# Performance work log

Hardware: AMD Instinct MI355X
Metric: run time of the kernel (lower is better)

Reference implementation:

```python
import jax, jax.numpy as jnp
import numpy as np

P = 16         # patch size
D = 192        # embed dim (vit_tiny)
NH = 3         # heads
DEPTH = 12
HID = 768      # mlp hidden = 4*D
NCLS = 1000
PCT = 0.25
EPS = 1e-6


def _ln(x, s, b):
    m = x.mean(-1, keepdims=True)
    v = ((x - m) ** 2).mean(-1, keepdims=True)
    return (x - m) * jax.lax.rsqrt(v + EPS) * s + b


def setup_inputs() -> dict:
    key = jax.random.key(0)
    ks = jax.random.split(key, 24)
    B, IMG = 64, 384
    std = 0.02
    d = {
        "magno_image": jax.random.normal(ks[0], (B, 3, IMG, IMG), jnp.float32),
        "line_drawing": jax.random.uniform(ks[1], (B, 1, IMG, IMG), jnp.float32),
        "conv_w": jax.random.normal(ks[2], (D, 3, P, P), jnp.float32) * std,
        "conv_b": jnp.zeros((D,), jnp.float32),
        "pos_embed": jax.random.normal(ks[3], (1, (IMG // P) ** 2 + 1, D), jnp.float32) * std,
        "cls_token": jax.random.normal(ks[4], (1, 1, D), jnp.float32) * std,
        "ln1_s": jnp.ones((DEPTH, D), jnp.float32),
        "ln1_b": jnp.zeros((DEPTH, D), jnp.float32),
        "qkv_w": jax.random.normal(ks[5], (DEPTH, D, 3 * D), jnp.float32) * std,
        "qkv_b": jnp.zeros((DEPTH, 3 * D), jnp.float32),
        "proj_w": jax.random.normal(ks[6], (DEPTH, D, D), jnp.float32) * std,
        "proj_b": jnp.zeros((DEPTH, D), jnp.float32),
        "ln2_s": jnp.ones((DEPTH, D), jnp.float32),
        "ln2_b": jnp.zeros((DEPTH, D), jnp.float32),
        "fc1_w": jax.random.normal(ks[7], (DEPTH, D, HID), jnp.float32) * std,
        "fc1_b": jnp.zeros((DEPTH, HID), jnp.float32),
        "fc2_w": jax.random.normal(ks[8], (DEPTH, HID, D), jnp.float32) * std,
        "fc2_b": jnp.zeros((DEPTH, D), jnp.float32),
        "normf_s": jnp.ones((D,), jnp.float32),
        "normf_b": jnp.zeros((D,), jnp.float32),
        "head_w": jax.random.normal(ks[9], (D, NCLS), jnp.float32) * std,
        "head_b": jnp.zeros((NCLS,), jnp.float32),
    }
    return d


def _forward(magno_image, line_drawing, conv_w, conv_b, pos_embed, cls_token,
             ln1_s, ln1_b, qkv_w, qkv_b, proj_w, proj_b, ln2_s, ln2_b,
             fc1_w, fc1_b, fc2_w, fc2_b, normf_s, normf_b, head_w, head_b):
    B, _, IMG, _ = magno_image.shape
    g = IMG // P
    N = g * g
    k = int(N * PCT)
    hd = D // NH

    # --- PatchImportanceScorer: avg-pool(patch_size) then flatten ---
    scores = line_drawing.reshape(B, g, P, g, P).mean(axis=(2, 4)).reshape(B, N)

    # --- patch embed (conv stride == kernel == reshaped matmul) ---
    x = magno_image.reshape(B, 3, g, P, g, P).transpose(0, 2, 4, 1, 3, 5)
    patches = x.reshape(B, N, 3 * P * P) @ conv_w.reshape(D, 3 * P * P).T + conv_b

    # --- top_k selection + gather of patches and pos-embed ---
    _, idx = jax.lax.top_k(scores, k)                      # (B, k)
    sel = jnp.take_along_axis(patches, idx[:, :, None], axis=1)
    pos = jnp.take_along_axis(
        jnp.broadcast_to(pos_embed[:, 1:, :], (B, N, D)), idx[:, :, None], axis=1)
    sel = sel + pos

    cls = jnp.broadcast_to(cls_token + pos_embed[:, :1, :], (B, 1, D))
    seq = jnp.concatenate([cls, sel], axis=1)              # (B, 1+k, D)
    S = 1 + k

    def block(h, p):
        l1s, l1b, qw, qb, pw, pb, l2s, l2b, f1w, f1b, f2w, f2b = p
        y = _ln(h, l1s, l1b)
        qkv = (y @ qw + qb).reshape(B, S, 3, NH, hd)
        q, kk, v = qkv[:, :, 0], qkv[:, :, 1], qkv[:, :, 2]  # (B,S,NH,hd)
        att = jnp.einsum('bqhd,bkhd->bhqk', q, kk) / np.sqrt(hd).astype(np.float32)
        att = jax.nn.softmax(att, axis=-1)
        o = jnp.einsum('bhqk,bkhd->bqhd', att, v).reshape(B, S, D)
        h = h + o @ pw + pb
        y = _ln(h, l2s, l2b)
        h = h + jax.nn.gelu(y @ f1w + f1b, approximate=False) @ f2w + f2b
        return h, None

    seq, _ = jax.lax.scan(block, seq, (ln1_s, ln1_b, qkv_w, qkv_b, proj_w, proj_b,
                                       ln2_s, ln2_b, fc1_w, fc1_b, fc2_w, fc2_b))
    seq = _ln(seq, normf_s, normf_b)
    return seq[:, 0] @ head_w + head_b


def reference(magno_image, line_drawing, conv_w, conv_b, pos_embed, cls_token,
              ln1_s, ln1_b, qkv_w, qkv_b, proj_w, proj_b, ln2_s, ln2_b,
              fc1_w, fc1_b, fc2_w, fc2_b, normf_s, normf_b, head_w, head_b):
    return _forward(magno_image, line_drawing, conv_w, conv_b, pos_embed, cls_token,
                    ln1_s, ln1_b, qkv_w, qkv_b, proj_w, proj_b, ln2_s, ln2_b,
                    fc1_w, fc1_b, fc2_w, fc2_b, normf_s, normf_b, head_w, head_b)
```

## Files before the change

kernel.cpp:

```cpp
#include <hip/hip_runtime.h>
#include <hip/hip_bf16.h>
#include <cmath>


#define Bsz   64
#define NPATCH 576
#define KSEL  144
#define SEQ   145
#define DIM   192
#define HIDN  768

typedef __bf16 bf16x8 __attribute__((ext_vector_type(8)));
typedef float  f32x4  __attribute__((ext_vector_type(4)));

__global__ __launch_bounds__(256) void scores_kernel(const float* __restrict__ line,
                                                     float* __restrict__ scores)
{
    int gp = blockIdx.x;
    int b = gp / NPATCH, p = gp % NPATCH;
    int gy = p / 24, gx = p % 24;
    int t = threadIdx.x, py = t >> 4, px = t & 15;
    float v = line[((size_t)b * 384 + gy * 16 + py) * 384 + gx * 16 + px];
    for (int off = 32; off; off >>= 1) v += __shfl_xor(v, off);
    __shared__ float red[4];
    if ((t & 63) == 0) red[t >> 6] = v;
    __syncthreads();
    if (t == 0) scores[gp] = (red[0] + red[1] + red[2] + red[3]) * (1.f / 256.f);
}

__global__ __launch_bounds__(256) void topk_kernel(const float* __restrict__ scores,
                                                   int* __restrict__ idx)
{
    int b = blockIdx.x;
    __shared__ float s[NPATCH];
    for (int i = threadIdx.x; i < NPATCH; i += 256) s[i] = scores[b * NPATCH + i];
    __syncthreads();
    for (int i = threadIdx.x; i < NPATCH; i += 256) {
        float si = s[i];
        int cnt = 0;
        for (int j = 0; j < NPATCH; ++j) {
            float sj = s[j];
            cnt += (sj > si) || (sj == si && j < i);
        }
        if (cnt < KSEL) idx[b * KSEL + cnt] = i;
    }
}

__global__ __launch_bounds__(256) void gather_kernel(const float* __restrict__ magno,
                                                     const int* __restrict__ idx,
                                                     __hip_bfloat16* __restrict__ selp)
{
    int bs = blockIdx.x;
    int b = bs / KSEL;
    int pi = idx[bs];
    int gy = pi / 24, gx = pi % 24;
    int t = threadIdx.x, py = t >> 4, px = t & 15;
    size_t src = ((size_t)b * 3 * 384 + gy * 16 + py) * 384 + gx * 16 + px;
    __hip_bfloat16* dst = &selp[(size_t)bs * 768];
#pragma unroll
    for (int c = 0; c < 3; ++c)
        dst[c * 256 + t] = __float2bfloat16(magno[src + (size_t)c * 384 * 384]);
}

__global__ __launch_bounds__(256) void convert_bf16_kernel(const float* __restrict__ src,
                                                           __hip_bfloat16* __restrict__ dst,
                                                           int n)
{
    int i = blockIdx.x * 256 + threadIdx.x;
    if (i < n) dst[i] = __float2bfloat16(src[i]);
}

__global__ __launch_bounds__(256) void transpose_w_kernel(const float* __restrict__ src,
                                                          __hip_bfloat16* __restrict__ dst,
                                                          int R, int C)
{
    __shared__ float t[32][33];
    size_t lo = (size_t)blockIdx.z * R * C;
    int r0 = blockIdx.y * 32, c0 = blockIdx.x * 32;
    int tx = threadIdx.x & 31, ty = threadIdx.x >> 5;
#pragma unroll
    for (int i = 0; i < 32; i += 8)
        t[ty + i][tx] = src[lo + (size_t)(r0 + ty + i) * C + c0 + tx];
    __syncthreads();
#pragma unroll
    for (int i = 0; i < 32; i += 8)
        dst[lo + (size_t)(c0 + ty + i) * R + r0 + tx] = __float2bfloat16(t[tx][ty + i]);
}

__global__ void cls_kernel(const float* __restrict__ cls, const float* __restrict__ pos,
                           float* __restrict__ h)
{
    int b = blockIdx.x, t = threadIdx.x;
    h[(size_t)b * SEQ * DIM + t] = cls[t] + pos[t];
}

__global__ __launch_bounds__(256) void ln_kernel(const float* __restrict__ x,
                                                 const float* __restrict__ s,
                                                 const float* __restrict__ bia,
                                                 __hip_bfloat16* __restrict__ y, int ntok)
{
    int w = threadIdx.x >> 6, lane = threadIdx.x & 63;
    int tok = blockIdx.x * 4 + w;
    if (tok >= ntok) return;
    const float* xp = &x[(size_t)tok * DIM];
    float x0 = xp[lane], x1 = xp[lane + 64], x2 = xp[lane + 128];
    float sum = x0 + x1 + x2;
    for (int off = 32; off; off >>= 1) sum += __shfl_xor(sum, off);
    float mean = sum * (1.f / 192.f);
    float d0 = x0 - mean, d1 = x1 - mean, d2 = x2 - mean;
    float vs = d0 * d0 + d1 * d1 + d2 * d2;
    for (int off = 32; off; off >>= 1) vs += __shfl_xor(vs, off);
    float rs = rsqrtf(vs * (1.f / 192.f) + 1e-6f);
    __hip_bfloat16* yp = &y[(size_t)tok * DIM];
    yp[lane]       = __float2bfloat16(d0 * rs * s[lane]       + bia[lane]);
    yp[lane + 64]  = __float2bfloat16(d1 * rs * s[lane + 64]  + bia[lane + 64]);
    yp[lane + 128] = __float2bfloat16(d2 * rs * s[lane + 128] + bia[lane + 128]);
}

template <int MODE>
__global__ __launch_bounds__(256) void gemm_bf16(const __hip_bfloat16* __restrict__ A,
                                                 const __hip_bfloat16* __restrict__ Wt,
                                                 const float* __restrict__ bias,
                                                 void* __restrict__ Cout,
                                                 int M, int N, int K,
                                                 const int* __restrict__ selidx,
                                                 const float* __restrict__ pos)
{
    __shared__ __align__(16) char As[8192];
    __shared__ __align__(16) char Bs[8192];
    const int tid = threadIdx.x;
    const int lane = tid & 63, wid = tid >> 6;
    const int wr = wid >> 1, wc = wid & 1;
    const int lr = lane & 15, lk = lane >> 4;
    const int m0 = blockIdx.y * 64, n0 = blockIdx.x * 64;
    f32x4 acc[2][2] = {};

    for (int k0 = 0; k0 < K; k0 += 64) {
#pragma unroll
        for (int it = 0; it < 2; ++it) {
            int chunk = it * 256 + tid;
            int r = chunk >> 3, g = chunk & 7;
            int loff = r * 128 + ((g ^ (r & 7)) * 16);
            *reinterpret_cast<uint4*>(As + loff) =
                *reinterpret_cast<const uint4*>(&A[(size_t)(m0 + r) * K + k0 + g * 8]);
            *reinterpret_cast<uint4*>(Bs + loff) =
                *reinterpret_cast<const uint4*>(&Wt[(size_t)(n0 + r) * K + k0 + g * 8]);
        }
        __syncthreads();
#pragma unroll
        for (int kc = 0; kc < 2; ++kc) {
            int g = kc * 4 + lk;
            bf16x8 af[2], bfr[2];
#pragma unroll
            for (int mi = 0; mi < 2; ++mi) {
                int r = wr * 32 + mi * 16 + lr;
                af[mi] = *reinterpret_cast<const bf16x8*>(As + r * 128 + ((g ^ (r & 7)) * 16));
            }
#pragma unroll
            for (int ni = 0; ni < 2; ++ni) {
                int r = wc * 32 + ni * 16 + lr;
                bfr[ni] = *reinterpret_cast<const bf16x8*>(Bs + r * 128 + ((g ^ (r & 7)) * 16));
            }
#pragma unroll
            for (int mi = 0; mi < 2; ++mi)
#pragma unroll
                for (int ni = 0; ni < 2; ++ni)
                    acc[mi][ni] = __builtin_amdgcn_mfma_f32_16x16x32_bf16(
                        af[mi], bfr[ni], acc[mi][ni], 0, 0, 0);
        }
        __syncthreads();
    }

#pragma unroll
    for (int mi = 0; mi < 2; ++mi)
#pragma unroll
    for (int ni = 0; ni < 2; ++ni)
#pragma unroll
    for (int j = 0; j < 4; ++j) {
        int row = m0 + wr * 32 + mi * 16 + (lane >> 4) * 4 + j;
        int col = n0 + wc * 32 + ni * 16 + (lane & 15);
        float v = acc[mi][ni][j] + bias[col];
        if (MODE == 2) {
            ((__hip_bfloat16*)Cout)[(size_t)row * N + col] =
                __float2bfloat16(0.5f * v * (1.f + erff(v * 0.70710678118654752f)));
        } else {
            int bb2 = row / KSEL, ss = row % KSEL;
            int pi = selidx[row];
            v += pos[(size_t)(1 + pi) * DIM + col];
            ((float*)Cout)[((size_t)bb2 * SEQ + 1 + ss) * DIM + col] = v;
        }
    }
}

__global__ __launch_bounds__(256) void gemm_qkv(const __hip_bfloat16* __restrict__ A,
                                                const __hip_bfloat16* __restrict__ Wt,
                                                const float* __restrict__ bias,
                                                __hip_bfloat16* __restrict__ qk,
                                                __hip_bfloat16* __restrict__ Vt)
{
    __shared__ __align__(16) char As[8192];
    __shared__ __align__(16) char Bs[8192];
    const int tid = threadIdx.x;
    const int lane = tid & 63, wid = tid >> 6;
    const int wr = wid >> 1, wc = wid & 1;
    const int lr = lane & 15, lk = lane >> 4;
    const int m0 = blockIdx.y * 64, n0 = blockIdx.x * 64;
    const int K = DIM;
    f32x4 acc[2][2] = {};

    for (int k0 = 0; k0 < K; k0 += 64) {
#pragma unroll
        for (int it = 0; it < 2; ++it) {
            int chunk = it * 256 + tid;
            int r = chunk >> 3, g = chunk & 7;
            int loff = r * 128 + ((g ^ (r & 7)) * 16);
            *reinterpret_cast<uint4*>(As + loff) =
                *reinterpret_cast<const uint4*>(&A[(size_t)(m0 + r) * K + k0 + g * 8]);
            *reinterpret_cast<uint4*>(Bs + loff) =
                *reinterpret_cast<const uint4*>(&Wt[(size_t)(n0 + r) * K + k0 + g * 8]);
        }
        __syncthreads();
#pragma unroll
        for (int kc = 0; kc < 2; ++kc) {
            int g = kc * 4 + lk;
            bf16x8 af[2], bfr[2];
#pragma unroll
            for (int mi = 0; mi < 2; ++mi) {
                int r = wr * 32 + mi * 16 + lr;
                af[mi] = *reinterpret_cast<const bf16x8*>(As + r * 128 + ((g ^ (r & 7)) * 16));
            }
#pragma unroll
            for (int ni = 0; ni < 2; ++ni) {
                int r = wc * 32 + ni * 16 + lr;
                bfr[ni] = *reinterpret_cast<const bf16x8*>(Bs + r * 128 + ((g ^ (r & 7)) * 16));
            }
#pragma unroll
            for (int mi = 0; mi < 2; ++mi)
#pragma unroll
                for (int ni = 0; ni < 2; ++ni)
                    acc[mi][ni] = __builtin_amdgcn_mfma_f32_16x16x32_bf16(
                        af[mi], bfr[ni], acc[mi][ni], 0, 0, 0);
        }
        __syncthreads();
    }

#pragma unroll
    for (int mi = 0; mi < 2; ++mi)
#pragma unroll
    for (int ni = 0; ni < 2; ++ni)
#pragma unroll
    for (int j = 0; j < 4; ++j) {
        int row = m0 + wr * 32 + mi * 16 + (lane >> 4) * 4 + j;
        int col = n0 + wc * 32 + ni * 16 + (lane & 15);
        float v = acc[mi][ni][j] + bias[col];
        if (col < 384) {
            qk[(size_t)row * 384 + col] = __float2bfloat16(v);
        } else {
            int c = col - 384;
            int b = row / SEQ, s = row - b * SEQ;
            Vt[((size_t)(b * 3 + (c >> 6)) * 64 + (c & 63)) * 160 + s] = __float2bfloat16(v);
        }
    }
}

__global__ __launch_bounds__(256) void attnproj_kernel(const __hip_bfloat16* __restrict__ qk,
                                                       const __hip_bfloat16* __restrict__ Vt,
                                                       const __hip_bfloat16* __restrict__ Wp,
                                                       const float* __restrict__ pbias,
                                                       float* __restrict__ h,
                                                       const float* __restrict__ ls,
                                                       const float* __restrict__ lb,
                                                       __hip_bfloat16* __restrict__ y)
{
    const int b = blockIdx.y, qt = blockIdx.x;
    const int tid = threadIdx.x;
    const int w = tid >> 6, lane = tid & 63;
    const int lr = lane & 15, lg = lane >> 4;
    __shared__ __hip_bfloat16 Ps[3][32][168];
    __shared__ __hip_bfloat16 Ot[32][200];
    __shared__ float redsum[4][32];
    __shared__ float redsq[4][32];

    const size_t qbase = (size_t)b * SEQ * 384;
    const int q0 = qt * 32;

    if (w < 3) {
        const int hh = w;
        bf16x8 aq[2][2];
#pragma unroll
        for (int mi = 0; mi < 2; ++mi)
#pragma unroll
            for (int ks = 0; ks < 2; ++ks)
                aq[mi][ks] = *reinterpret_cast<const bf16x8*>(
                    &qk[qbase + (size_t)(q0 + mi * 16 + lr) * 384 + hh * 64 + ks * 32 + lg * 8]);
        f32x4 sc[2][10];
#pragma unroll
        for (int mi = 0; mi < 2; ++mi)
#pragma unroll
            for (int nf = 0; nf < 10; ++nf) sc[mi][nf] = (f32x4){0.f, 0.f, 0.f, 0.f};
#pragma unroll
        for (int nf = 0; nf < 10; ++nf) {
            int key = nf * 16 + lr;
#pragma unroll
            for (int ks = 0; ks < 2; ++ks) {
                bf16x8 bk = *reinterpret_cast<const bf16x8*>(
                    &qk[qbase + (size_t)key * 384 + 192 + hh * 64 + ks * 32 + lg * 8]);
#pragma unroll
                for (int mi = 0; mi < 2; ++mi)
                    sc[mi][nf] = __builtin_amdgcn_mfma_f32_16x16x32_bf16(
                        aq[mi][ks], bk, sc[mi][nf], 0, 0, 0);
            }
        }
#pragma unroll
        for (int mi = 0; mi < 2; ++mi) {
            float mx[4] = {-1e30f, -1e30f, -1e30f, -1e30f};
#pragma unroll
            for (int nf = 0; nf < 10; ++nf) {
                bool valid = nf * 16 + lr < SEQ;
#pragma unroll
                for (int j = 0; j < 4; ++j) {
                    float v = valid ? sc[mi][nf][j] * 0.125f : -1e30f;
                    sc[mi][nf][j] = v;
                    mx[j] = fmaxf(mx[j], v);
                }
            }
#pragma unroll
            for (int j = 0; j < 4; ++j)
                for (int off = 1; off < 16; off <<= 1)
                    mx[j] = fmaxf(mx[j], __shfl_xor(mx[j], off));
            float sm[4] = {0.f, 0.f, 0.f, 0.f};
#pragma unroll
            for (int nf = 0; nf < 10; ++nf)
#pragma unroll
                for (int j = 0; j < 4; ++j) {
                    float p = __expf(sc[mi][nf][j] - mx[j]);
                    sc[mi][nf][j] = p;
                    sm[j] += p;
                }
#pragma unroll
            for (int j = 0; j < 4; ++j) {
                for (int off = 1; off < 16; off <<= 1) sm[j] += __shfl_xor(sm[j], off);
                sm[j] = 1.f / sm[j];
            }
#pragma unroll
            for (int nf = 0; nf < 10; ++nf) {
                int key = nf * 16 + lr;
#pragma unroll
                for (int j = 0; j < 4; ++j)
                    Ps[hh][mi * 16 + lg * 4 + j][key] = __float2bfloat16(sc[mi][nf][j] * sm[j]);
            }
        }
        const __hip_bfloat16* vtb = &Vt[(size_t)(b * 3 + hh) * 64 * 160];
        f32x4 oacc[2][4];
#pragma unroll
        for (int mi = 0; mi < 2; ++mi)
#pragma unroll
            for (int nf = 0; nf < 4; ++nf) oacc[mi][nf] = (f32x4){0.f, 0.f, 0.f, 0.f};
#pragma unroll
        for (int ks = 0; ks < 5; ++ks) {
            bf16x8 ap[2];
            ap[0] = *reinterpret_cast<const bf16x8*>(&Ps[hh][lr][ks * 32 + lg * 8]);
            ap[1] = *reinterpret_cast<const bf16x8*>(&Ps[hh][16 + lr][ks * 32 + lg * 8]);
#pragma unroll
            for (int nf = 0; nf < 4; ++nf) {
                bf16x8 bv = *reinterpret_cast<const bf16x8*>(
                    &vtb[(size_t)(nf * 16 + lr) * 160 + ks * 32 + lg * 8]);
#pragma unroll
                for (int mi = 0; mi < 2; ++mi)
                    oacc[mi][nf] = __builtin_amdgcn_mfma_f32_16x16x32_bf16(
                        ap[mi], bv, oacc[mi][nf], 0, 0, 0);
            }
        }
#pragma unroll
        for (int mi = 0; mi < 2; ++mi)
#pragma unroll
            for (int nf = 0; nf < 4; ++nf)
#pragma unroll
                for (int j = 0; j < 4; ++j)
                    Ot[mi * 16 + lg * 4 + j][hh * 64 + nf * 16 + lr] =
                        __float2bfloat16(oacc[mi][nf][j]);
    }
    __syncthreads();

    f32x4 pacc[2][3];
#pragma unroll
    for (int mi = 0; mi < 2; ++mi)
#pragma unroll
        for (int nf = 0; nf < 3; ++nf) pacc[mi][nf] = (f32x4){0.f, 0.f, 0.f, 0.f};
#pragma unroll
    for (int kk = 0; kk < 6; ++kk) {
        bf16x8 af[2];
        af[0] = *reinterpret_cast<const bf16x8*>(&Ot[lr][kk * 32 + lg * 8]);
        af[1] = *reinterpret_cast<const bf16x8*>(&Ot[16 + lr][kk * 32 + lg * 8]);
#pragma unroll
        for (int nf = 0; nf < 3; ++nf) {
            int ncol = w * 48 + nf * 16 + lr;
            bf16x8 bw = *reinterpret_cast<const bf16x8*>(&Wp[(size_t)ncol * 192 + kk * 32 + lg * 8]);
#pragma unroll
            for (int mi = 0; mi < 2; ++mi)
                pacc[mi][nf] = __builtin_amdgcn_mfma_f32_16x16x32_bf16(
                    af[mi], bw, pacc[mi][nf], 0, 0, 0);
        }
    }
    float v[2][3][4];
    float psum[2][4] = {}, psq[2][4] = {};
#pragma unroll
    for (int mi = 0; mi < 2; ++mi)
#pragma unroll
    for (int nf = 0; nf < 3; ++nf) {
        int col = w * 48 + nf * 16 + lr;
        float bcol = pbias[col];
#pragma unroll
        for (int j = 0; j < 4; ++j) {
            int q = q0 + mi * 16 + lg * 4 + j;
            float res = (q < SEQ) ? h[((size_t)b * SEQ + q) * DIM + col] : 0.f;
            float t = pacc[mi][nf][j] + bcol + res;
            v[mi][nf][j] = t;
            psum[mi][j] += t;
            psq[mi][j] += t * t;
        }
    }
#pragma unroll
    for (int mi = 0; mi < 2; ++mi)
#pragma unroll
        for (int j = 0; j < 4; ++j) {
            for (int off = 1; off < 16; off <<= 1) {
                psum[mi][j] += __shfl_xor(psum[mi][j], off);
                psq[mi][j]  += __shfl_xor(psq[mi][j], off);
            }
            redsum[w][mi * 16 + lg * 4 + j] = psum[mi][j];
            redsq[w][mi * 16 + lg * 4 + j]  = psq[mi][j];
        }
    __syncthreads();
#pragma unroll
    for (int mi = 0; mi < 2; ++mi) {
#pragma unroll
        for (int j = 0; j < 4; ++j) {
            int r = mi * 16 + lg * 4 + j;
            int q = q0 + r;
            if (q >= SEQ) continue;
            float tsum = redsum[0][r] + redsum[1][r] + redsum[2][r] + redsum[3][r];
            float tsq  = redsq[0][r]  + redsq[1][r]  + redsq[2][r]  + redsq[3][r];
            float mean = tsum * (1.f / 192.f);
            float var  = tsq * (1.f / 192.f) - mean * mean;
            float rs = rsqrtf(var + 1e-6f);
#pragma unroll
            for (int nf = 0; nf < 3; ++nf) {
                int col = w * 48 + nf * 16 + lr;
                float t = v[mi][nf][j];
                h[((size_t)b * SEQ + q) * DIM + col] = t;
                y[((size_t)b * SEQ + q) * DIM + col] =
                    __float2bfloat16((t - mean) * rs * ls[col] + lb[col]);
            }
        }
    }
}

template <bool DO_LN>
__global__ __launch_bounds__(256) void gemm_res_ln32(const __hip_bfloat16* __restrict__ A,
                                                     const __hip_bfloat16* __restrict__ Wt,
                                                     const float* __restrict__ bias,
                                                     float* __restrict__ h,
                                                     const float* __restrict__ ls,
                                                     const float* __restrict__ lb,
                                                     __hip_bfloat16* __restrict__ y)
{
    __shared__ __align__(16) char As[4096];
    __shared__ __align__(16) char Bs[24576];
    __shared__ float redsum[2][32];
    __shared__ float redsq[2][32];
    const int tid = threadIdx.x;
    const int lane = tid & 63, w = tid >> 6;
    const int wm = w & 1, wn = w >> 1;
    const int lr = lane & 15, lg = lane >> 4;
    const int m0 = blockIdx.x * 32;
    const int K = HIDN;
    f32x4 acc[6] = {};

    for (int k0 = 0; k0 < K; k0 += 64) {
        {
            int r = tid >> 3, g = tid & 7;
            *reinterpret_cast<uint4*>(As + r * 128 + ((g ^ (r & 7)) * 16)) =
                *reinterpret_cast<const uint4*>(&A[(size_t)(m0 + r) * K + k0 + g * 8]);
        }
        {
            int chunk = tid;
#pragma unroll
            for (int it = 0; it < 6; ++it, chunk += 256) {
                int r = chunk >> 3, g = chunk & 7;
                *reinterpret_cast<uint4*>(Bs + r * 128 + ((g ^ (r & 7)) * 16)) =
                    *reinterpret_cast<const uint4*>(&Wt[(size_t)r * K + k0 + g * 8]);
            }
        }
        __syncthreads();
#pragma unroll
        for (int kc = 0; kc < 2; ++kc) {
            int g = kc * 4 + lg;
            int ar = wm * 16 + lr;
            bf16x8 af = *reinterpret_cast<const bf16x8*>(As + ar * 128 + ((g ^ (ar & 7)) * 16));
#pragma unroll
            for (int nf = 0; nf < 6; ++nf) {
                int br = wn * 96 + nf * 16 + lr;
                bf16x8 bfv = *reinterpret_cast<const bf16x8*>(Bs + br * 128 + ((g ^ (br & 7)) * 16));
                acc[nf] = __builtin_amdgcn_mfma_f32_16x16x32_bf16(af, bfv, acc[nf], 0, 0, 0);
            }
        }
        __syncthreads();
    }

    float v[6][4];
    float sum[4] = {0.f, 0.f, 0.f, 0.f}, sq[4] = {0.f, 0.f, 0.f, 0.f};
#pragma unroll
    for (int nf = 0; nf < 6; ++nf) {
        int col = wn * 96 + nf * 16 + lr;
        float bcol = bias[col];
#pragma unroll
        for (int j = 0; j < 4; ++j) {
            int row = m0 + wm * 16 + lg * 4 + j;
            float t = acc[nf][j] + bcol + h[(size_t)row * DIM + col];
            v[nf][j] = t;
            sum[j] += t;
            sq[j] += t * t;
        }
    }
    if (DO_LN) {
#pragma unroll
        for (int j = 0; j < 4; ++j) {
            for (int off = 1; off < 16; off <<= 1) {
                sum[j] += __shfl_xor(sum[j], off);
                sq[j]  += __shfl_xor(sq[j], off);
            }
            if (lr == 0) {
                redsum[wn][wm * 16 + lg * 4 + j] = sum[j];
                redsq[wn][wm * 16 + lg * 4 + j]  = sq[j];
            }
        }
        __syncthreads();
#pragma unroll
        for (int j = 0; j < 4; ++j) {
            int r = wm * 16 + lg * 4 + j;
            int row = m0 + r;
            float tsum = redsum[0][r] + redsum[1][r];
            float tsq  = redsq[0][r]  + redsq[1][r];
            float mean = tsum * (1.f / 192.f);
            float var  = tsq * (1.f / 192.f) - mean * mean;
            float rs = rsqrtf(var + 1e-6f);
#pragma unroll
            for (int nf = 0; nf < 6; ++nf) {
                int col = wn * 96 + nf * 16 + lr;
                float t = v[nf][j];
                h[(size_t)row * DIM + col] = t;
                y[(size_t)row * DIM + col] =
                    __float2bfloat16((t - mean) * rs * ls[col] + lb[col]);
            }
        }
    } else {
#pragma unroll
        for (int nf = 0; nf < 6; ++nf) {
            int col = wn * 96 + nf * 16 + lr;
#pragma unroll
            for (int j = 0; j < 4; ++j) {
                int row = m0 + wm * 16 + lg * 4 + j;
                h[(size_t)row * DIM + col] = v[nf][j];
            }
        }
    }
}

__global__ __launch_bounds__(256) void head_kernel(const float* __restrict__ h,
                                                   const float* __restrict__ nfs,
                                                   const float* __restrict__ nfb,
                                                   const float* __restrict__ hw,
                                                   const float* __restrict__ hb,
                                                   float* __restrict__ out)
{
    int b = blockIdx.x, t = threadIdx.x;
    __shared__ float y[DIM];
    __shared__ float red[4];
    float x = (t < DIM) ? h[(size_t)b * SEQ * DIM + t] : 0.f;
    float sum = x;
    for (int off = 32; off; off >>= 1) sum += __shfl_xor(sum, off);
    if ((t & 63) == 0) red[t >> 6] = sum;
    __syncthreads();
    float mean = (red[0] + red[1] + red[2] + red[3]) * (1.f / 192.f);
    __syncthreads();
    float d = (t < DIM) ? (x - mean) : 0.f;
    float v = d * d;
    for (int off = 32; off; off >>= 1) v += __shfl_xor(v, off);
    if ((t & 63) == 0) red[t >> 6] = v;
    __syncthreads();
    float var = (red[0] + red[1] + red[2] + red[3]) * (1.f / 192.f);
    float rs = rsqrtf(var + 1e-6f);
    if (t < DIM) y[t] = d * rs * nfs[t] + nfb[t];
    __syncthreads();
    for (int n = t; n < 1000; n += 256) {
        float acc = hb[n];
#pragma unroll 8
        for (int k = 0; k < DIM; ++k)
            acc = fmaf(y[k], hw[(size_t)k * 1000 + n], acc);
        out[(size_t)b * 1000 + n] = acc;
    }
}

extern "C" void kernel_launch(void* const* d_in, const int* in_sizes, int n_in,
                              void* d_out, int out_size, void* d_ws, size_t ws_size,
                              hipStream_t stream)
{
    const float* magno  = (const float*)d_in[0];
    const float* line   = (const float*)d_in[1];
    const float* conv_w = (const float*)d_in[2];
    const float* conv_b = (const float*)d_in[3];
    const float* pos    = (const float*)d_in[4];
    const float* cls    = (const float*)d_in[5];
    const float* ln1_s  = (const float*)d_in[6];
    const float* ln1_b  = (const float*)d_in[7];
    const float* qkv_w  = (const float*)d_in[8];
    const float* qkv_b  = (const float*)d_in[9];
    const float* proj_w = (const float*)d_in[10];
    const float* proj_b = (const float*)d_in[11];
    const float* ln2_s  = (const float*)d_in[12];
    const float* ln2_b  = (const float*)d_in[13];
    const float* fc1_w  = (const float*)d_in[14];
    const float* fc1_b  = (const float*)d_in[15];
    const float* fc2_w  = (const float*)d_in[16];
    const float* fc2_b  = (const float*)d_in[17];
    const float* normf_s = (const float*)d_in[18];
    const float* normf_b = (const float*)d_in[19];
    const float* head_w = (const float*)d_in[20];
    const float* head_b = (const float*)d_in[21];
    float* out = (float*)d_out;
    (void)in_sizes; (void)n_in; (void)out_size; (void)ws_size;

    char* ws = (char*)d_ws;
    int*            idx     = (int*)            (ws + 0);
    float*          h       = (float*)          (ws + 147456);
    __hip_bfloat16* y       = (__hip_bfloat16*) (ws + 7274496);
    __hip_bfloat16* qk      = (__hip_bfloat16*) (ws + 10838016);
    __hip_bfloat16* Vt      = (__hip_bfloat16*) (ws + 17965056);
    __hip_bfloat16* tbuf    = (__hip_bfloat16*) (ws + 21897216);
    __hip_bfloat16* wt_qkv  = (__hip_bfloat16*) (ws + 36151296);
    __hip_bfloat16* wt_proj = (__hip_bfloat16*) (ws + 38805504);
    __hip_bfloat16* wt_fc1  = (__hip_bfloat16*) (ws + 39690240);
    __hip_bfloat16* wt_fc2  = (__hip_bfloat16*) (ws + 43229184);
    float*          scoresbuf = (float*)qk;
    __hip_bfloat16* convT     = y;
    __hip_bfloat16* selp      = tbuf;

    hipMemsetAsync(Vt, 0, 3932160, stream);
    transpose_w_kernel<<<dim3(18, 6, 12), 256, 0, stream>>>(qkv_w, wt_qkv, DIM, 576);
    transpose_w_kernel<<<dim3(6, 6, 12),  256, 0, stream>>>(proj_w, wt_proj, DIM, DIM);
    transpose_w_kernel<<<dim3(24, 6, 12), 256, 0, stream>>>(fc1_w, wt_fc1, DIM, HIDN);
    transpose_w_kernel<<<dim3(6, 24, 12), 256, 0, stream>>>(fc2_w, wt_fc2, HIDN, DIM);
    convert_bf16_kernel<<<576, 256, 0, stream>>>(conv_w, convT, DIM * 768);

    scores_kernel<<<Bsz * NPATCH, 256, 0, stream>>>(line, scoresbuf);
    topk_kernel<<<Bsz, 256, 0, stream>>>(scoresbuf, idx);
    gather_kernel<<<Bsz * KSEL, 256, 0, stream>>>(magno, idx, selp);
    cls_kernel<<<Bsz, DIM, 0, stream>>>(cls, pos, h);
    gemm_bf16<3><<<dim3(3, 144), 256, 0, stream>>>(selp, convT, conv_b, h,
                                                   9216, DIM, 768, idx, pos);

    const int ntok = Bsz * SEQ;
    ln_kernel<<<ntok / 4, 256, 0, stream>>>(h, ln1_s, ln1_b, y, ntok);
    for (int l = 0; l < 12; ++l) {
        gemm_qkv<<<dim3(9, 145), 256, 0, stream>>>(y, wt_qkv + (size_t)l * 576 * DIM,
                                                   qkv_b + l * 576, qk, Vt);
        attnproj_kernel<<<dim3(5, Bsz), 256, 0, stream>>>(qk, Vt,
                                                          wt_proj + (size_t)l * DIM * DIM,
                                                          proj_b + l * DIM, h,
                                                          ln2_s + l * DIM, ln2_b + l * DIM, y);
        gemm_bf16<2><<<dim3(12, 145), 256, 0, stream>>>(y, wt_fc1 + (size_t)l * HIDN * DIM,
                                                        fc1_b + l * HIDN, tbuf,
                                                        ntok, HIDN, DIM, nullptr, nullptr);
        if (l < 11)
            gemm_res_ln32<true><<<ntok / 32, 256, 0, stream>>>(
                tbuf, wt_fc2 + (size_t)l * DIM * HIDN, fc2_b + l * DIM, h,
                ln1_s + (l + 1) * DIM, ln1_b + (l + 1) * DIM, y);
        else
            gemm_res_ln32<false><<<ntok / 32, 256, 0, stream>>>(
                tbuf, wt_fc2 + (size_t)l * DIM * HIDN, fc2_b + l * DIM, h,
                nullptr, nullptr, y);
    }
    head_kernel<<<Bsz, 256, 0, stream>>>(h, normf_s, normf_b, head_w, head_b, out);
}
```

Measured before the change: 1.136 ms.

## Widen attention and fc2 residual-LN kernels to 512 threads with retiled work

The attention+projection kernel now runs 8 waves instead of 4. Each of the 6 attention waves handles one head and one 16-query half, and the projection is split 2x4 across all 8 waves. The fc2 GEMM with residual and LayerNorm now uses 64-row tiles, 512 threads and a 128-wide K step, which cuts the grid from 290 to 145 blocks. The goal is more parallel waves per block and fewer redundant weight loads per row. The cost is larger shared-memory use (about 64KB) and lower block count, which may limit occupancy on the CUs.

```diff
diff --git a/kernel.cpp b/kernel.cpp
--- a/kernel.cpp
+++ b/kernel.cpp
@@ -263,7 +263,7 @@
     }
 }
 
-__global__ __launch_bounds__(256) void attnproj_kernel(const __hip_bfloat16* __restrict__ qk,
+__global__ __launch_bounds__(512) void attnproj_kernel(const __hip_bfloat16* __restrict__ qk,
                                                        const __hip_bfloat16* __restrict__ Vt,
                                                        const __hip_bfloat16* __restrict__ Wp,
                                                        const float* __restrict__ pbias,
@@ -284,20 +284,15 @@
     const size_t qbase = (size_t)b * SEQ * 384;
     const int q0 = qt * 32;
 
-    if (w < 3) {
-        const int hh = w;
-        bf16x8 aq[2][2];
-#pragma unroll
-        for (int mi = 0; mi < 2; ++mi)
-#pragma unroll
-            for (int ks = 0; ks < 2; ++ks)
-                aq[mi][ks] = *reinterpret_cast<const bf16x8*>(
-                    &qk[qbase + (size_t)(q0 + mi * 16 + lr) * 384 + hh * 64 + ks * 32 + lg * 8]);
-        f32x4 sc[2][10];
-#pragma unroll
-        for (int mi = 0; mi < 2; ++mi)
-#pragma unroll
-            for (int nf = 0; nf < 10; ++nf) sc[mi][nf] = (f32x4){0.f, 0.f, 0.f, 0.f};
+    if (w < 6) {
+        const int hh = w >> 1, half = w & 1;
+        const int qrow = q0 + half * 16;
+        bf16x8 aq[2];
+#pragma unroll
+        for (int ks = 0; ks < 2; ++ks)
+            aq[ks] = *reinterpret_cast<const bf16x8*>(
+                &qk[qbase + (size_t)(qrow + lr) * 384 + hh * 64 + ks * 32 + lg * 8]);
+        f32x4 sc[10] = {};
 #pragma unroll
         for (int nf = 0; nf < 10; ++nf) {
             int key = nf * 16 + lr;
@@ -305,263 +300,248 @@
             for (int ks = 0; ks < 2; ++ks) {
                 bf16x8 bk = *reinterpret_cast<const bf16x8*>(
                     &qk[qbase + (size_t)key * 384 + 192 + hh * 64 + ks * 32 + lg * 8]);
-#pragma unroll
-                for (int mi = 0; mi < 2; ++mi)
-                    sc[mi][nf] = __builtin_amdgcn_mfma_f32_16x16x32_bf16(
-                        aq[mi][ks], bk, sc[mi][nf], 0, 0, 0);
-            }
-        }
-#pragma unroll
-        for (int mi = 0; mi < 2; ++mi) {
-            float mx[4] = {-1e30f, -1e30f, -1e30f, -1e30f};
-#pragma unroll
-            for (int nf = 0; nf < 10; ++nf) {
-                bool valid = nf * 16 + lr < SEQ;
-#pragma unroll
-                for (int j = 0; j < 4; ++j) {
-                    float v = valid ? sc[mi][nf][j] * 0.125f : -1e30f;
-                    sc[mi][nf][j] = v;
-                    mx[j] = fmaxf(mx[j], v);
-                }
-            }
+                sc[nf] = __builtin_amdgcn_mfma_f32_16x16x32_bf16(aq[ks], bk, sc[nf], 0, 0, 0);
+            }
+        }
+        float mx[4] = {-1e30f, -1e30f, -1e30f, -1e30f};
+#pragma unroll
+        for (int nf = 0; nf < 10; ++nf) {
+            bool valid = nf * 16 + lr < SEQ;
+#pragma unroll
+            for (int j = 0; j < 4; ++j) {
+                float v = valid ? sc[nf][j] * 0.125f : -1e30f;
+                sc[nf][j] = v;
+                mx[j] = fmaxf(mx[j], v);
+            }
+        }
+#pragma unroll
+        for (int j = 0; j < 4; ++j)
+            for (int off = 1; off < 16; off <<= 1)
+                mx[j] = fmaxf(mx[j], __shfl_xor(mx[j], off));
+        float sm[4] = {0.f, 0.f, 0.f, 0.f};
+#pragma unroll
+        for (int nf = 0; nf < 10; ++nf)
+#pragma unroll
+            for (int j = 0; j < 4; ++j) {
+                float p = __expf(sc[nf][j] - mx[j]);
+                sc[nf][j] = p;
+                sm[j] += p;
+            }
+#pragma unroll
+        for (int j = 0; j < 4; ++j) {
+            for (int off = 1; off < 16; off <<= 1) sm[j] += __shfl_xor(sm[j], off);
+            sm[j] = 1.f / sm[j];
+        }
+#pragma unroll
+        for (int nf = 0; nf < 10; ++nf) {
+            int key = nf * 16 + lr;
 #pragma unroll
             for (int j = 0; j < 4; ++j)
-                for (int off = 1; off < 16; off <<= 1)
-                    mx[j] = fmaxf(mx[j], __shfl_xor(mx[j], off));
-            float sm[4] = {0.f, 0.f, 0.f, 0.f};
-#pragma unroll
-            for (int nf = 0; nf < 10; ++nf)
-#pragma unroll
-                for (int j = 0; j < 4; ++j) {
-                    float p = __expf(sc[mi][nf][j] - mx[j]);
-                    sc[mi][nf][j] = p;
-                    sm[j] += p;
-                }
-#pragma unroll
-            for (int j = 0; j < 4; ++j) {
-                for (int off = 1; off < 16; off <<= 1) sm[j] += __shfl_xor(sm[j], off);
-                sm[j] = 1.f / sm[j];
-            }
-#pragma unroll
-            for (int nf = 0; nf < 10; ++nf) {
-                int key = nf * 16 + lr;
-#pragma unroll
-                for (int j = 0; j < 4; ++j)
-                    Ps[hh][mi * 16 + lg * 4 + j][key] = __float2bfloat16(sc[mi][nf][j] * sm[j]);
-            }
+                Ps[hh][half * 16 + lg * 4 + j][key] = __float2bfloat16(sc[nf][j] * sm[j]);
         }
         const __hip_bfloat16* vtb = &Vt[(size_t)(b * 3 + hh) * 64 * 160];
-        f32x4 oacc[2][4];
-#pragma unroll
-        for (int mi = 0; mi < 2; ++mi)
-#pragma unroll
-            for (int nf = 0; nf < 4; ++nf) oacc[mi][nf] = (f32x4){0.f, 0.f, 0.f, 0.f};
+        f32x4 oacc[4] = {};
 #pragma unroll
         for (int ks = 0; ks < 5; ++ks) {
-            bf16x8 ap[2];
-            ap[0] = *reinterpret_cast<const bf16x8*>(&Ps[hh][lr][ks * 32 + lg * 8]);
-            ap[1] = *reinterpret_cast<const bf16x8*>(&Ps[hh][16 + lr][ks * 32 + lg * 8]);
+            bf16x8 ap = *reinterpret_cast<const bf16x8*>(&Ps[hh][half * 16 + lr][ks * 32 + lg * 8]);
 #pragma unroll
             for (int nf = 0; nf < 4; ++nf) {
                 bf16x8 bv = *reinterpret_cast<const bf16x8*>(
                     &vtb[(size_t)(nf * 16 + lr) * 160 + ks * 32 + lg * 8]);
-#pragma unroll
-                for (int mi = 0; mi < 2; ++mi)
-                    oacc[mi][nf] = __builtin_amdgcn_mfma_f32_16x16x32_bf16(
-                        ap[mi], bv, oacc[mi][nf], 0, 0, 0);
-            }
-        }
-#pragma unroll
-        for (int mi = 0; mi < 2; ++mi)
-#pragma unroll
-            for (int nf = 0; nf < 4; ++nf)
-#pragma unroll
-                for (int j = 0; j < 4; ++j)
-                    Ot[mi * 16 + lg * 4 + j][hh * 64 + nf * 16 + lr] =
-                        __float2bfloat16(oacc[mi][nf][j]);
-    }
-    __syncthreads();
-
-    f32x4 pacc[2][3];
-#pragma unroll
-    for (int mi = 0; mi < 2; ++mi)
-#pragma unroll
-        for (int nf = 0; nf < 3; ++nf) pacc[mi][nf] = (f32x4){0.f, 0.f, 0.f, 0.f};
+                oacc[nf] = __builtin_amdgcn_mfma_f32_16x16x32_bf16(ap, bv, oacc[nf], 0, 0, 0);
+            }
+        }
+#pragma unroll
+        for (int nf = 0; nf < 4; ++nf)
+#pragma unroll
+            for (int j = 0; j < 4; ++j)
+                Ot[half * 16 + lg * 4 + j][hh * 64 + nf * 16 + lr] =
+                    __float2bfloat16(oacc[nf][j]);
+    }
+    __syncthreads();
+
+    const int wm = w & 1, wn = w >> 1;
+    f32x4 pacc[3] = {};
 #pragma unroll
     for (int kk = 0; kk < 6; ++kk) {
-        bf16x8 af[2];
-        af[0] = *reinterpret_cast<const bf16x8*>(&Ot[lr][kk * 32 + lg * 8]);
-        af[1] = *reinterpret_cast<const bf16x8*>(&Ot[16 + lr][kk * 32 + lg * 8]);
+        bf16x8 af = *reinterpret_cast<const bf16x8*>(&Ot[wm * 16 + lr][kk * 32 + lg * 8]);
 #pragma unroll
         for (int nf = 0; nf < 3; ++nf) {
-            int ncol = w * 48 + nf * 16 + lr;
+            int ncol = wn * 48 + nf * 16 + lr;
             bf16x8 bw = *reinterpret_cast<const bf16x8*>(&Wp[(size_t)ncol * 192 + kk * 32 + lg * 8]);
-#pragma unroll
-            for (int mi = 0; mi < 2; ++mi)
-                pacc[mi][nf] = __builtin_amdgcn_mfma_f32_16x16x32_bf16(
-                    af[mi], bw, pacc[mi][nf], 0, 0, 0);
-        }
-    }
-    float v[2][3][4];
-    float psum[2][4] = {}, psq[2][4] = {};
-#pragma unroll
-    for (int mi = 0; mi < 2; ++mi)
+            pacc[nf] = __builtin_amdgcn_mfma_f32_16x16x32_bf16(af, bw, pacc[nf], 0, 0, 0);
+        }
+    }
+    float v[3][4];
+    float psum[4] = {}, psq[4] = {};
 #pragma unroll
     for (int nf = 0; nf < 3; ++nf) {
-        int col = w * 48 + nf * 16 + lr;
+        int col = wn * 48 + nf * 16 + lr;
         float bcol = pbias[col];
 #pragma unroll
         for (int j = 0; j < 4; ++j) {
-            int q = q0 + mi * 16 + lg * 4 + j;
+            int q = q0 + wm * 16 + lg * 4 + j;
             float res = (q < SEQ) ? h[((size_t)b * SEQ + q) * DIM + col] : 0.f;
-            float t = pacc[mi][nf][j] + bcol + res;
-            v[mi][nf][j] = t;
-            psum[mi][j] += t;
-            psq[mi][j] += t * t;
-        }
-    }
-#pragma unroll
-    for (int mi = 0; mi < 2; ++mi)
-#pragma unroll
-        for (int j = 0; j < 4; ++j) {
-            for (int off = 1; off < 16; off <<= 1) {
-                psum[mi][j] += __shfl_xor(psum[mi][j], off);
-                psq[mi][j]  += __shfl_xor(psq[mi][j], off);
-            }
-            redsum[w][mi * 16 + lg * 4 + j] = psum[mi][j];
-            redsq[w][mi * 16 + lg * 4 + j]  = psq[mi][j];
-        }
-    __syncthreads();
-#pragma unroll
-    for (int mi = 0; mi < 2; ++mi) {
-#pragma unroll
-        for (int j = 0; j < 4; ++j) {
-            int r = mi * 16 + lg * 4 + j;
-            int q = q0 + r;
-            if (q >= SEQ) continue;
-            float tsum = redsum[0][r] + redsum[1][r] + redsum[2][r] + redsum[3][r];
-            float tsq  = redsq[0][r]  + redsq[1][r]  + redsq[2][r]  + redsq[3][r];
-            float mean = tsum * (1.f / 192.f);
-            float var  = tsq * (1.f / 192.f) - mean * mean;
-            float rs = rsqrtf(var + 1e-6f);
-#pragma unroll
-            for (int nf = 0; nf < 3; ++nf) {
-                int col = w * 48 + nf * 16 + lr;
-                float t = v[mi][nf][j];
-                h[((size_t)b * SEQ + q) * DIM + col] = t;
-                y[((size_t)b * SEQ + q) * DIM + col] =
-                    __float2bfloat16((t - mean) * rs * ls[col] + lb[col]);
-            }
+            float t = pacc[nf][j] + bcol + res;
+            v[nf][j] = t;
+            psum[j] += t;
+            psq[j] += t * t;
+        }
+    }
+#pragma unroll
+    for (int j = 0; j < 4; ++j) {
+        for (int off = 1; off < 16; off <<= 1) {
+            psum[j] += __shfl_xor(psum[j], off);
+            psq[j]  += __shfl_xor(psq[j], off);
+        }
+        if (lr == 0) {
+            redsum[wn][wm * 16 + lg * 4 + j] = psum[j];
+            redsq[wn][wm * 16 + lg * 4 + j]  = psq[j];
+        }
+    }
+    __syncthreads();
+#pragma unroll
+    for (int j = 0; j < 4; ++j) {
+        int r = wm * 16 + lg * 4 + j;
+        int q = q0 + r;
+        if (q >= SEQ) continue;
+        float tsum = redsum[0][r] + redsum[1][r] + redsum[2][r] + redsum[3][r];
+        float tsq  = redsq[0][r]  + redsq[1][r]  + redsq[2][r]  + redsq[3][r];
+        float mean = tsum * (1.f / 192.f);
+        float var  = tsq * (1.f / 192.f) - mean * mean;
+        float rs = rsqrtf(var + 1e-6f);
+#pragma unroll
+        for (int nf = 0; nf < 3; ++nf) {
+            int col = wn * 48 + nf * 16 + lr;
+            float t = v[nf][j];
+            h[((size_t)b * SEQ + q) * DIM + col] = t;
+            y[((size_t)b * SEQ + q) * DIM + col] =
+                __float2bfloat16((t - mean) * rs * ls[col] + lb[col]);
         }
     }
 }
 
 template <bool DO_LN>
-__global__ __launch_bounds__(256) void gemm_res_ln32(const __hip_bfloat16* __restrict__ A,
-                                                     const __hip_bfloat16* __restrict__ Wt,
-                                                     const float* __restrict__ bias,
-                                                     float* __restrict__ h,
-                                                     const float* __restrict__ ls,
-                                                     const float* __restrict__ lb,
-                                                     __hip_bfloat16* __restrict__ y)
-{
-    __shared__ __align__(16) char As[4096];
-    __shared__ __align__(16) char Bs[24576];
-    __shared__ float redsum[2][32];
-    __shared__ float redsq[2][32];
+__global__ __launch_bounds__(512) void gemm_res_ln(const __hip_bfloat16* __restrict__ A,
+                                                   const __hip_bfloat16* __restrict__ Wt,
+                                                   const float* __restrict__ bias,
+                                                   float* __restrict__ h,
+                                                   const float* __restrict__ ls,
+                                                   const float* __restrict__ lb,
+                                                   __hip_bfloat16* __restrict__ y,
+                                                   int K)
+{
+    __shared__ __align__(16) char As[16384];
+    __shared__ __align__(16) char Bs[49152];
+    __shared__ float redsum[4][64];
+    __shared__ float redsq[4][64];
     const int tid = threadIdx.x;
     const int lane = tid & 63, w = tid >> 6;
     const int wm = w & 1, wn = w >> 1;
     const int lr = lane & 15, lg = lane >> 4;
-    const int m0 = blockIdx.x * 32;
-    const int K = HIDN;
-    f32x4 acc[6] = {};
-
-    for (int k0 = 0; k0 < K; k0 += 64) {
-        {
-            int r = tid >> 3, g = tid & 7;
-            *reinterpret_cast<uint4*>(As + r * 128 + ((g ^ (r & 7)) * 16)) =
+    const int m0 = blockIdx.x * 64;
+    f32x4 acc[2][3] = {};
+
+    for (int k0 = 0; k0 < K; k0 += 128) {
+#pragma unroll
+        for (int it = 0; it < 2; ++it) {
+            int chunk = it * 512 + tid;
+            int r = chunk >> 4, g = chunk & 15;
+            *reinterpret_cast<uint4*>(As + r * 256 + ((g ^ (r & 15)) * 16)) =
                 *reinterpret_cast<const uint4*>(&A[(size_t)(m0 + r) * K + k0 + g * 8]);
         }
-        {
-            int chunk = tid;
-#pragma unroll
-            for (int it = 0; it < 6; ++it, chunk += 256) {
-                int r = chunk >> 3, g = chunk & 7;
-                *reinterpret_cast<uint4*>(Bs + r * 128 + ((g ^ (r & 7)) * 16)) =
-                    *reinterpret_cast<const uint4*>(&Wt[(size_t)r * K + k0 + g * 8]);
-            }
+#pragma unroll
+        for (int it = 0; it < 6; ++it) {
+            int chunk = it * 512 + tid;
+            int r = chunk >> 4, g = chunk & 15;
+            *reinterpret_cast<uint4*>(Bs + r * 256 + ((g ^ (r & 15)) * 16)) =
+                *reinterpret_cast<const uint4*>(&Wt[(size_t)r * K + k0 + g * 8]);
         }
         __syncthreads();
 #pragma unroll
-        for (int kc = 0; kc < 2; ++kc) {
+        for (int kc = 0; kc < 4; ++kc) {
             int g = kc * 4 + lg;
-            int ar = wm * 16 + lr;
-            bf16x8 af = *reinterpret_cast<const bf16x8*>(As + ar * 128 + ((g ^ (ar & 7)) * 16));
-#pragma unroll
-            for (int nf = 0; nf < 6; ++nf) {
-                int br = wn * 96 + nf * 16 + lr;
-                bf16x8 bfv = *reinterpret_cast<const bf16x8*>(Bs + br * 128 + ((g ^ (br & 7)) * 16));
-                acc[nf] = __builtin_amdgcn_mfma_f32_16x16x32_bf16(af, bfv, acc[nf], 0, 0, 0);
+            bf16x8 af[2];
+#pragma unroll
+            for (int mi = 0; mi < 2; ++mi) {
+                int r = wm * 32 + mi * 16 + lr;
+                af[mi] = *reinterpret_cast<const bf16x8*>(As + r * 256 + ((g ^ (r & 15)) * 16));
+            }
+#pragma unroll
+            for (int nf = 0; nf < 3; ++nf) {
+                int br = wn * 48 + nf * 16 + lr;
+                bf16x8 bw = *reinterpret_cast<const bf16x8*>(Bs + br * 256 + ((g ^ (br & 15)) * 16));
+#pragma unroll
+                for (int mi = 0; mi < 2; ++mi)
+                    acc[mi][nf] = __builtin_amdgcn_mfma_f32_16x16x32_bf16(
+                        af[mi], bw, acc[mi][nf], 0, 0, 0);
             }
         }
         __syncthreads();
     }
 
-    float v[6][4];
-    float sum[4] = {0.f, 0.f, 0.f, 0.f}, sq[4] = {0.f, 0.f, 0.f, 0.f};
-#pragma unroll
-    for (int nf = 0; nf < 6; ++nf) {
-        int col = wn * 96 + nf * 16 + lr;
+    float v[2][3][4];
+    float psum[2][4] = {}, psq[2][4] = {};
+#pragma unroll
+    for (int mi = 0; mi < 2; ++mi)
+#pragma unroll
+    for (int nf = 0; nf < 3; ++nf) {
+        int col = wn * 48 + nf * 16 + lr;
         float bcol = bias[col];
 #pragma unroll
         for (int j = 0; j < 4; ++j) {
-            int row = m0 + wm * 16 + lg * 4 + j;
-            float t = acc[nf][j] + bcol + h[(size_t)row * DIM + col];
-            v[nf][j] = t;
-            sum[j] += t;
-            sq[j] += t * t;
+            int row = m0 + wm * 32 + mi * 16 + lg * 4 + j;
+            float t = acc[mi][nf][j] + bcol + h[(size_t)row * DIM + col];
+            v[mi][nf][j] = t;
+            psum[mi][j] += t;
+            psq[mi][j] += t * t;
         }
     }
     if (DO_LN) {
 #pragma unroll
-        for (int j = 0; j < 4; ++j) {
-            for (int off = 1; off < 16; off <<= 1) {
-                sum[j] += __shfl_xor(sum[j], off);
-                sq[j]  += __shfl_xor(sq[j], off);
-            }
-            if (lr == 0) {
-                redsum[wn][wm * 16 + lg * 4 + j] = sum[j];
-                redsq[wn][wm * 16 + lg * 4 + j]  = sq[j];
-            }
-        }
+        for (int mi = 0; mi < 2; ++mi)
+#pragma unroll
+            for (int j = 0; j < 4; ++j) {
+                for (int off = 1; off < 16; off <<= 1) {
+                    psum[mi][j] += __shfl_xor(psum[mi][j], off);
+                    psq[mi][j]  += __shfl_xor(psq[mi][j], off);
+                }
+                if (lr == 0) {
+                    redsum[wn][wm * 32 + mi * 16 + lg * 4 + j] = psum[mi][j];
+                    redsq[wn][wm * 32 + mi * 16 + lg * 4 + j]  = psq[mi][j];
+                }
+            }
         __syncthreads();
 #pragma unroll
-        for (int j = 0; j < 4; ++j) {
-            int r = wm * 16 + lg * 4 + j;
-            int row = m0 + r;
-            float tsum = redsum[0][r] + redsum[1][r];
-            float tsq  = redsq[0][r]  + redsq[1][r];
-            float mean = tsum * (1.f / 192.f);
-            float var  = tsq * (1.f / 192.f) - mean * mean;
-            float rs = rsqrtf(var + 1e-6f);
-#pragma unroll
-            for (int nf = 0; nf < 6; ++nf) {
-                int col = wn * 96 + nf * 16 + lr;
-                float t = v[nf][j];
-                h[(size_t)row * DIM + col] = t;
-                y[(size_t)row * DIM + col] =
-                    __float2bfloat16((t - mean) * rs * ls[col] + lb[col]);
-            }
-        }
+        for (int mi = 0; mi < 2; ++mi)
+#pragma unroll
+            for (int j = 0; j < 4; ++j) {
+                int r = wm * 32 + mi * 16 + lg * 4 + j;
+                int row = m0 + r;
+                float tsum = redsum[0][r] + redsum[1][r] + redsum[2][r] + redsum[3][r];
+                float tsq  = redsq[0][r]  + redsq[1][r]  + redsq[2][r]  + redsq[3][r];
+                float mean = tsum * (1.f / 192.f);
+                float var  = tsq * (1.f / 192.f) - mean * mean;
+                float rs = rsqrtf(var + 1e-6f);
+#pragma unroll
+                for (int nf = 0; nf < 3; ++nf) {
+                    int col = wn * 48 + nf * 16 + lr;
+                    float t = v[mi][nf][j];
+                    h[(size_t)row * DIM + col] = t;
+                    y[(size_t)row * DIM + col] =
+                        __float2bfloat16((t - mean) * rs * ls[col] + lb[col]);
+                }
+            }
     } else {
 #pragma unroll
-        for (int nf = 0; nf < 6; ++nf) {
-            int col = wn * 96 + nf * 16 + lr;
+        for (int mi = 0; mi < 2; ++mi)
+#pragma unroll
+        for (int nf = 0; nf < 3; ++nf) {
+            int col = wn * 48 + nf * 16 + lr;
 #pragma unroll
             for (int j = 0; j < 4; ++j) {
-                int row = m0 + wm * 16 + lg * 4 + j;
-                h[(size_t)row * DIM + col] = v[nf][j];
+                int row = m0 + wm * 32 + mi * 16 + lg * 4 + j;
+                h[(size_t)row * DIM + col] = v[mi][nf][j];
             }
         }
     }
@@ -665,7 +645,7 @@
     for (int l = 0; l < 12; ++l) {
         gemm_qkv<<<dim3(9, 145), 256, 0, stream>>>(y, wt_qkv + (size_t)l * 576 * DIM,
                                                    qkv_b + l * 576, qk, Vt);
-        attnproj_kernel<<<dim3(5, Bsz), 256, 0, stream>>>(qk, Vt,
+        attnproj_kernel<<<dim3(5, Bsz), 512, 0, stream>>>(qk, Vt,
                                                           wt_proj + (size_t)l * DIM * DIM,
                                                           proj_b + l * DIM, h,
                                                           ln2_s + l * DIM, ln2_b + l * DIM, y);
@@ -673,13 +653,13 @@
                                                         fc1_b + l * HIDN, tbuf,
                                                         ntok, HIDN, DIM, nullptr, nullptr);
         if (l < 11)
-            gemm_res_ln32<true><<<ntok / 32, 256, 0, stream>>>(
+            gemm_res_ln<true><<<145, 512, 0, stream>>>(
                 tbuf, wt_fc2 + (size_t)l * DIM * HIDN, fc2_b + l * DIM, h,
-                ln1_s + (l + 1) * DIM, ln1_b + (l + 1) * DIM, y);
+                ln1_s + (l + 1) * DIM, ln1_b + (l + 1) * DIM, y, HIDN);
         else
-            gemm_res_ln32<false><<<ntok / 32, 256, 0, stream>>>(
+            gemm_res_ln<false><<<145, 512, 0, stream>>>(
                 tbuf, wt_fc2 + (size_t)l * DIM * HIDN, fc2_b + l * DIM, h,
-                nullptr, nullptr, y);
+                nullptr, nullptr, y, HIDN);
     }
     head_kernel<<<Bsz, 256, 0, stream>>>(h, normf_s, normf_b, head_w, head_b, out);
 }
```

Measured after the change: 967.3 us. -14.9%, faster.
